# Optimization experiments

Measured on AMD Instinct MI355X. Metric: run time of the kernel, lower is better.

## Reference

```python
import jax, jax.numpy as jnp
import numpy as np

NUM_HEADS = 16
ROPE_THETA = 10000.0


def _rotate_half(x):
    d = x.shape[-1] // 2
    return jnp.concatenate((-x[..., d:], x[..., :d]), axis=-1)


def setup_inputs() -> dict:
    key = jax.random.key(0)
    k1, k2, k3, k4 = jax.random.split(key, 4)
    T, HID = 3072, 1024
    hidden_states = jax.random.normal(k1, (T, HID), dtype=jnp.float32)
    w_qkv = jax.random.normal(k2, (HID, 3 * HID), dtype=jnp.float32) * (1.0 / np.sqrt(HID))
    w_o = jax.random.normal(k3, (HID, HID), dtype=jnp.float32) * (1.0 / np.sqrt(HID))
    attention_mask = jnp.zeros((T, T), dtype=jnp.float32)  # additive bias over token pairs
    position_ids = jax.random.randint(k4, (T,), 0, T, dtype=jnp.int32)
    return {
        "hidden_states": hidden_states,
        "w_qkv": w_qkv,
        "w_o": w_o,
        "attention_mask": attention_mask,
        "position_ids": position_ids,
    }


def reference(hidden_states, w_qkv, w_o, attention_mask, position_ids):
    T, hid = hidden_states.shape
    H = NUM_HEADS
    D = hid // H

    # fused QKV projection (bias=False)
    qkv = hidden_states @ w_qkv  # [T, 3*hid]
    q, k, v = jnp.split(qkv, 3, axis=-1)
    q = q.reshape(T, H, D)
    k = k.reshape(T, H, D)
    v = v.reshape(T, H, D)

    # RoPE per packed-token position_ids
    inv_freq = 1.0 / (ROPE_THETA ** (jnp.arange(0, D, 2, dtype=jnp.float32) / D))  # [D/2]
    freqs = position_ids.astype(jnp.float32)[:, None] * inv_freq[None, :]  # [T, D/2]
    emb = jnp.concatenate((freqs, freqs), axis=-1)  # [T, D]
    cos = jnp.cos(emb)[:, None, :]  # [T, 1, D]
    sin = jnp.sin(emb)[:, None, :]
    q = q * cos + _rotate_half(q) * sin
    k = k * cos + _rotate_half(k) * sin

    # dense token-token attention over packed tokens
    scale = 1.0 / np.sqrt(D).astype(np.float32)
    scores = jnp.einsum("thd,shd->hts", q, k) * scale  # [H, T, T]
    scores = scores + attention_mask[None, :, :]
    probs = jax.nn.softmax(scores, axis=-1)
    out = jnp.einsum("hts,shd->thd", probs, v).reshape(T, hid)
    return out @ w_o
```

## Files before the change

### kernel.cpp

```cpp
#include <hip/hip_runtime.h>
#include <hip/hip_bf16.h>
#include <hip/hip_fp16.h>
#include <math.h>

#define T_TOK 3072
#define HID   1024
#define NH    16
#define HD    64
#define KVSPLIT 4
#define KVCHUNK (T_TOK / KVSPLIT)
#define NQB (T_TOK / 128)
#define LOG2E 1.4426950408889634f

typedef __attribute__((ext_vector_type(8))) short bf16x8;
typedef __attribute__((ext_vector_type(8))) unsigned short u16x8;
typedef __attribute__((ext_vector_type(4))) float f32x4;
typedef __attribute__((ext_vector_type(16))) float f32x16;
typedef __attribute__((ext_vector_type(4))) unsigned int u32x4;

#define VMCNT(n) asm volatile("s_waitcnt vmcnt(" #n ")" ::: "memory")
#define SB() __builtin_amdgcn_sched_barrier(0)

static __device__ __forceinline__ unsigned short f2bf(float x) {
  __hip_bfloat16 h = __float2bfloat16(x);
  return __builtin_bit_cast(unsigned short, h);
}
static __device__ __forceinline__ float bf2f(unsigned short u) {
  unsigned int v = (unsigned int)u << 16;
  return __builtin_bit_cast(float, v);
}
static __device__ __forceinline__ unsigned short f2h(float x) {
  __half h = __float2half(x);
  return __builtin_bit_cast(unsigned short, h);
}
static __device__ __forceinline__ float h2f(unsigned short u) {
  __half h = __builtin_bit_cast(__half, u);
  return __half2float(h);
}
static __device__ __forceinline__ unsigned int pack_bf16(float a, float b) {
  unsigned int ua = __builtin_bit_cast(unsigned int, a) + 0x8000u;
  unsigned int ub = __builtin_bit_cast(unsigned int, b) + 0x8000u;
  return (ua >> 16) | (ub & 0xffff0000u);
}

static __device__ __forceinline__ int swz(int row, int cb) {
  return row * 64 + ((cb ^ ((row & 7) << 4)) >> 1);
}

__global__ __launch_bounds__(256) void prep(const float* __restrict__ X,
                                            const float* __restrict__ Wqkv,
                                            const float* __restrict__ Wo,
                                            const int* __restrict__ pos,
                                            const float* __restrict__ mask,
                                            unsigned short* __restrict__ Xb,
                                            unsigned short* __restrict__ WqkvT,
                                            unsigned short* __restrict__ WoT,
                                            float* __restrict__ ctab,
                                            float* __restrict__ stab,
                                            int* __restrict__ flags) {
  __shared__ float tile[32][33];
  __shared__ int sflag;
  const int b = blockIdx.x;
  const int tid = threadIdx.x;
  if (b < 3072) {
    int i = (b * 256 + tid) * 4;
    float4 v = *(const float4*)(X + i);
    ushort4 o;
    o.x = f2bf(v.x); o.y = f2bf(v.y); o.z = f2bf(v.z); o.w = f2bf(v.w);
    *(ushort4*)(Xb + i) = o;
  } else if (b < 6144) {
    int b2 = b - 3072;
    int c0 = (b2 % 96) * 32, r0 = (b2 / 96) * 32;
    int tx = tid & 31, ty = tid >> 5;
    #pragma unroll
    for (int i2 = 0; i2 < 32; i2 += 8)
      tile[ty + i2][tx] = Wqkv[(size_t)(r0 + ty + i2) * 3072 + c0 + tx];
    __syncthreads();
    #pragma unroll
    for (int i2 = 0; i2 < 32; i2 += 8)
      WqkvT[(size_t)(c0 + ty + i2) * 1024 + r0 + tx] = f2bf(tile[tx][ty + i2]);
  } else if (b < 7168) {
    int b2 = b - 6144;
    int c0 = (b2 % 32) * 32, r0 = (b2 / 32) * 32;
    int tx = tid & 31, ty = tid >> 5;
    #pragma unroll
    for (int i2 = 0; i2 < 32; i2 += 8)
      tile[ty + i2][tx] = Wo[(size_t)(r0 + ty + i2) * 1024 + c0 + tx];
    __syncthreads();
    #pragma unroll
    for (int i2 = 0; i2 < 32; i2 += 8)
      WoT[(size_t)(c0 + ty + i2) * 1024 + r0 + tx] = f2bf(tile[tx][ty + i2]);
  } else if (b < 7552) {
    int i = (b - 7168) * 256 + tid;
    int t = i >> 5, j = i & 31;
    float inv = expf(-(float)j * 0.28782313662425572f);
    float f = (float)pos[t] * inv;
    ctab[i] = cosf(f);
    stab[i] = sinf(f);
  } else {
    int c = b - 7552;
    int qx = c % NQB, z = c / NQB;
    const float* base = mask + (size_t)(qx * 128) * T_TOK + z * KVCHUNK;
    int any = 0;
    const int NC4 = KVCHUNK / 4;
    for (int i = tid; i < 128 * NC4; i += 256) {
      int row = i / NC4, cc = i - row * NC4;
      float4 v = *(const float4*)(base + (size_t)row * T_TOK + cc * 4);
      any |= (v.x != 0.f) | (v.y != 0.f) | (v.z != 0.f) | (v.w != 0.f);
    }
    if (tid == 0) sflag = 0;
    __syncthreads();
    if (__any(any) && (tid & 63) == 0) sflag = 1;
    __syncthreads();
    if (tid == 0) flags[z * NQB + qx] = sflag;
  }
}

__global__ __launch_bounds__(256) void rope_v(const unsigned short* __restrict__ QKVb,
                                              const float* __restrict__ ctab,
                                              const float* __restrict__ stab,
                                              unsigned short* __restrict__ Qh,
                                              unsigned short* __restrict__ Kh,
                                              unsigned short* __restrict__ Vt) {
  const float QSCL = 0.18033688011112042f;
  const int h = blockIdx.y;
  const int t0 = blockIdx.x * 64;
  const int g = threadIdx.x & 3, tl = threadIdx.x >> 2;
  const int t = t0 + tl;
  __shared__ unsigned short vlds[64][72];

  const size_t rowb = (size_t)t * (3 * HID) + h * HD + g * 8;
  u16x8 qa = *(const u16x8*)(QKVb + rowb);
  u16x8 qb = *(const u16x8*)(QKVb + rowb + 32);
  u16x8 ka = *(const u16x8*)(QKVb + rowb + HID);
  u16x8 kb = *(const u16x8*)(QKVb + rowb + HID + 32);
  u16x8 va = *(const u16x8*)(QKVb + rowb + 2 * HID);
  u16x8 vb = *(const u16x8*)(QKVb + rowb + 2 * HID + 32);

  u16x8 qo0, qo1, ko0, ko1;
  #pragma unroll
  for (int e = 0; e < 8; ++e) {
    int j = g * 8 + e;
    float c = ctab[t * 32 + j], s = stab[t * 32 + j];
    float q1 = bf2f(qa[e]), q2 = bf2f(qb[e]);
    float k1 = bf2f(ka[e]), k2 = bf2f(kb[e]);
    qo0[e] = f2bf((q1 * c - q2 * s) * QSCL);
    qo1[e] = f2bf((q2 * c + q1 * s) * QSCL);
    ko0[e] = f2bf(k1 * c - k2 * s);
    ko1[e] = f2bf(k2 * c + k1 * s);
    vlds[tl][j] = va[e];
    vlds[tl][32 + j] = vb[e];
  }
  size_t ob = ((size_t)h * T_TOK + t) * HD + g * 8;
  *(u16x8*)(Qh + ob) = qo0;
  *(u16x8*)(Qh + ob + 32) = qo1;
  *(u16x8*)(Kh + ob) = ko0;
  *(u16x8*)(Kh + ob + 32) = ko1;

  __syncthreads();
  u16x8 o0, o1;
  #pragma unroll
  for (int e = 0; e < 8; ++e) {
    o0[e] = vlds[g * 16 + e][tl];
    o1[e] = vlds[g * 16 + 8 + e][tl];
  }
  u16x8 w0, w1;
  #pragma unroll
  for (int e = 0; e < 4; ++e) {
    w0[e] = o0[e];     w0[4 + e] = o1[e];
    w1[e] = o0[4 + e]; w1[4 + e] = o1[4 + e];
  }
  size_t vb2 = ((size_t)h * HD + tl) * T_TOK + t0 + g * 16;
  *(u16x8*)(Vt + vb2) = w0;
  *(u16x8*)(Vt + vb2 + 8) = w1;
}

template <int OBF16>
__device__ __forceinline__ void gemm_body(const unsigned short* __restrict__ A,
                                          const unsigned short* __restrict__ Bt,
                                          float* __restrict__ C,
                                          unsigned short* __restrict__ Cb,
                                          int M, int N, int K) {
  __shared__ unsigned short As[2][128 * 32];
  __shared__ unsigned short Bs[2][128 * 32];
  const int lane = threadIdx.x & 63;
  const int wv = threadIdx.x >> 6;
  const int wm = wv >> 1, wn = wv & 1;
  const int r = lane & 15, hi = lane >> 4;
  const int nwg = gridDim.x;
  const int flat = blockIdx.x;
  const int sid = (flat & 7) * (nwg >> 3) + (flat >> 3);
  const int mblocks = M >> 7;
  const int m0 = (sid % mblocks) * 128, n0 = (sid / mblocks) * 128;

  const int srow = lane >> 2;
  const int scb  = ((lane & 3) * 16) ^ ((srow & 3) << 4);
  const unsigned short* ga = A  + (size_t)(m0 + wv * 16 + srow) * K + (scb >> 1);
  const unsigned short* gb = Bt + (size_t)(n0 + wv * 16 + srow) * K + (scb >> 1);
  char* asd = (char*)&As[0][0] + wv * 1024;
  char* bsd = (char*)&Bs[0][0] + wv * 1024;

  auto stage = [&](int buf, int kt) {
    __builtin_amdgcn_global_load_lds(
        (const __attribute__((address_space(1))) unsigned int*)(ga + kt),
        (__attribute__((address_space(3))) unsigned int*)(asd + buf * 8192), 16, 0, 0);
    __builtin_amdgcn_global_load_lds(
        (const __attribute__((address_space(1))) unsigned int*)(ga + (size_t)64 * K + kt),
        (__attribute__((address_space(3))) unsigned int*)(asd + buf * 8192 + 4096), 16, 0, 0);
    __builtin_amdgcn_global_load_lds(
        (const __attribute__((address_space(1))) unsigned int*)(gb + kt),
        (__attribute__((address_space(3))) unsigned int*)(bsd + buf * 8192), 16, 0, 0);
    __builtin_amdgcn_global_load_lds(
        (const __attribute__((address_space(1))) unsigned int*)(gb + (size_t)64 * K + kt),
        (__attribute__((address_space(3))) unsigned int*)(bsd + buf * 8192 + 4096), 16, 0, 0);
  };

  f32x4 acc[4][4] = {};
  const int NT = K >> 5;
  stage(0, 0);
  #pragma unroll 2
  for (int it = 0; it < NT; ++it) {
    const int buf = it & 1;
    if (it + 1 < NT) {
      stage(buf ^ 1, (it + 1) * 32);
      VMCNT(4);
    } else {
      VMCNT(0);
    }
    SB();
    __builtin_amdgcn_s_barrier();
    SB();
    bf16x8 a[4], b[4];
    const int cbs = (hi * 16) ^ ((r & 3) << 4);
    #pragma unroll
    for (int tm = 0; tm < 4; ++tm)
      a[tm] = *(const bf16x8*)&As[buf][(wm * 64 + tm * 16 + r) * 32 + (cbs >> 1)];
    #pragma unroll
    for (int tn = 0; tn < 4; ++tn)
      b[tn] = *(const bf16x8*)&Bs[buf][(wn * 64 + tn * 16 + r) * 32 + (cbs >> 1)];
    #pragma unroll
    for (int tm = 0; tm < 4; ++tm)
      #pragma unroll
      for (int tn = 0; tn < 4; ++tn)
        acc[tm][tn] = __builtin_amdgcn_mfma_f32_16x16x32_bf16(a[tm], b[tn], acc[tm][tn], 0, 0, 0);
    __builtin_amdgcn_s_barrier();
  }
  #pragma unroll
  for (int tm = 0; tm < 4; ++tm)
    #pragma unroll
    for (int tn = 0; tn < 4; ++tn) {
      int colg = n0 + wn * 64 + tn * 16 + r;
      int rowg = m0 + wm * 64 + tm * 16 + hi * 4;
      if (OBF16) {
        unsigned short* cp = Cb + (size_t)rowg * N + colg;
        #pragma unroll
        for (int j = 0; j < 4; ++j) cp[(size_t)j * N] = f2bf(acc[tm][tn][j]);
      } else {
        float* cp = C + (size_t)rowg * N + colg;
        #pragma unroll
        for (int j = 0; j < 4; ++j) cp[(size_t)j * N] = acc[tm][tn][j];
      }
    }
}

__global__ __launch_bounds__(256) void gemm_bt(const unsigned short* __restrict__ A,
                                               const unsigned short* __restrict__ Bt,
                                               float* __restrict__ C, int M, int N, int K) {
  gemm_body<0>(A, Bt, C, nullptr, M, N, K);
}
__global__ __launch_bounds__(256) void gemm_bt_bf16(const unsigned short* __restrict__ A,
                                                    const unsigned short* __restrict__ Bt,
                                                    unsigned short* __restrict__ Cb,
                                                    int M, int N, int K) {
  gemm_body<1>(A, Bt, nullptr, Cb, M, N, K);
}

__global__ __launch_bounds__(256) void flash_attn(const unsigned short* __restrict__ Qh,
                                                  const unsigned short* __restrict__ Kh,
                                                  const unsigned short* __restrict__ Vt,
                                                  const float* __restrict__ mask,
                                                  const int* __restrict__ flags,
                                                  unsigned short* __restrict__ Op,
                                                  float* __restrict__ Mp,
                                                  float* __restrict__ Lp) {
  const int NBLK = NH * NQB * KVSPLIT;
  int id = blockIdx.x;
  int sid = (id & 7) * (NBLK / 8) + (id >> 3);
  const int hh = sid / (NQB * KVSPLIT);
  int rem = sid % (NQB * KVSPLIT);
  const int z  = rem / NQB;
  const int qx = rem % NQB;
  const int q0 = qx * 128;
  const int kv0 = z * KVCHUNK;
  const int NT = KVCHUNK / 64;

  __shared__ unsigned short Ks[2][64 * 64];
  __shared__ unsigned short Vs[2][64 * 64];
  const int lane = threadIdx.x & 63, wv = threadIdx.x >> 6;
  const int q31 = lane & 31, h2 = lane >> 5;
  const int qw = q0 + wv * 32 + q31;

  bf16x8 qf[4];
  #pragma unroll
  for (int ks = 0; ks < 4; ++ks)
    qf[ks] = *(const bf16x8*)(Qh + ((size_t)hh * T_TOK + qw) * HD + ks * 16 + h2 * 8);

  f32x16 acc_o[2] = {};
  const int hasmask = flags[z * NQB + qx];
  float m = hasmask ? -INFINITY : 0.f;
  float l = 0.f;

  const int ldrow = lane >> 3;
  const int colS  = ((lane & 7) * 16) ^ (ldrow << 4);
  const unsigned short* kga = Kh + ((size_t)hh * T_TOK + wv * 16 + ldrow) * HD + (colS >> 1);
  const unsigned short* vga = Vt + ((size_t)hh * HD + wv * 16 + ldrow) * T_TOK + (colS >> 1);
  char* ksd = (char*)&Ks[0][0] + wv * 2048;
  char* vsd = (char*)&Vs[0][0] + wv * 2048;
  const float* mrow = mask + (size_t)qw * T_TOK;

  auto stage = [&](int buf, int s0) {
    __builtin_amdgcn_global_load_lds(
        (const __attribute__((address_space(1))) unsigned int*)(kga + (size_t)s0 * HD),
        (__attribute__((address_space(3))) unsigned int*)(ksd + buf * 8192), 16, 0, 0);
    __builtin_amdgcn_global_load_lds(
        (const __attribute__((address_space(1))) unsigned int*)(kga + (size_t)s0 * HD + 8 * HD),
        (__attribute__((address_space(3))) unsigned int*)(ksd + buf * 8192 + 1024), 16, 0, 0);
    __builtin_amdgcn_global_load_lds(
        (const __attribute__((address_space(1))) unsigned int*)(vga + s0),
        (__attribute__((address_space(3))) unsigned int*)(vsd + buf * 8192), 16, 0, 0);
    __builtin_amdgcn_global_load_lds(
        (const __attribute__((address_space(1))) unsigned int*)(vga + s0 + 8 * T_TOK),
        (__attribute__((address_space(3))) unsigned int*)(vsd + buf * 8192 + 1024), 16, 0, 0);
  };

  float4 mk[8];

  auto qkt = [&](int cur, f32x16& as0, f32x16& as1) {
    __builtin_amdgcn_s_setprio(1);
    #pragma unroll
    for (int ks = 0; ks < 4; ++ks) {
      bf16x8 kf0 = *(const bf16x8*)&Ks[cur][swz(q31,      ks * 32 + h2 * 16)];
      bf16x8 kf1 = *(const bf16x8*)&Ks[cur][swz(32 + q31, ks * 32 + h2 * 16)];
      as0 = __builtin_amdgcn_mfma_f32_32x32x16_bf16(kf0, qf[ks], as0, 0, 0, 0);
      as1 = __builtin_amdgcn_mfma_f32_32x32x16_bf16(kf1, qf[ks], as1, 0, 0, 0);
    }
    __builtin_amdgcn_s_setprio(0);
  };

  auto pv = [&](int cur, const unsigned int* pk) {
    __builtin_amdgcn_s_setprio(1);
    #pragma unroll
    for (int kvb = 0; kvb < 2; ++kvb)
      #pragma unroll
      for (int s = 0; s < 2; ++s) {
        u32x4 fr;
        fr[0] = pk[kvb * 8 + 4 * s + 0];
        fr[1] = pk[kvb * 8 + 4 * s + 1];
        fr[2] = pk[kvb * 8 + 4 * s + 2];
        fr[3] = pk[kvb * 8 + 4 * s + 3];
        bf16x8 pfrag = __builtin_bit_cast(bf16x8, fr);
        #pragma unroll
        for (int db = 0; db < 2; ++db) {
          bf16x8 vf = *(const bf16x8*)&Vs[cur][swz(db * 32 + q31, kvb * 64 + s * 32 + h2 * 16)];
          acc_o[db] = __builtin_amdgcn_mfma_f32_32x32x16_bf16(vf, pfrag, acc_o[db], 0, 0, 0);
        }
      }
    __builtin_amdgcn_s_setprio(0);
  };

  auto tile_nomask = [&](int cur) {
    f32x16 as0 = {}, as1 = {};
    qkt(cur, as0, as1);
    float ps = 0.f;
    unsigned int pk[16];
    #pragma unroll
    for (int kvb = 0; kvb < 2; ++kvb) {
      const f32x16& as = kvb ? as1 : as0;
      #pragma unroll
      for (int j = 0; j < 4; ++j) {
        float e0 = __builtin_amdgcn_exp2f(as[j * 4 + 0]);
        float e1 = __builtin_amdgcn_exp2f(as[j * 4 + 1]);
        float e2 = __builtin_amdgcn_exp2f(as[j * 4 + 2]);
        float e3 = __builtin_amdgcn_exp2f(as[j * 4 + 3]);
        ps += (e0 + e1) + (e2 + e3);
        pk[kvb * 8 + j * 2 + 0] = pack_bf16(e0, e1);
        pk[kvb * 8 + j * 2 + 1] = pack_bf16(e2, e3);
      }
    }
    l += ps;
    pv(cur, pk);
  };

  auto tile_mask = [&](int cur) {
    f32x16 as0 = {}, as1 = {};
    qkt(cur, as0, as1);
    float sv[2][16];
    #pragma unroll
    for (int reg = 0; reg < 16; ++reg) {
      float m0v = (&mk[0 + (reg >> 2)].x)[reg & 3];
      float m1v = (&mk[4 + (reg >> 2)].x)[reg & 3];
      sv[0][reg] = fmaf(m0v, LOG2E, as0[reg]);
      sv[1][reg] = fmaf(m1v, LOG2E, as1[reg]);
    }
    float p0 = sv[0][0];
    #pragma unroll
    for (int i = 1; i < 16; ++i) p0 = fmaxf(p0, sv[0][i]);
    #pragma unroll
    for (int i = 0; i < 16; ++i) p0 = fmaxf(p0, sv[1][i]);
    float pmax = fmaxf(p0, __shfl_xor(p0, 32));
    if (__any(pmax > m + 8.f)) {
      float mnew = fmaxf(m, pmax);
      float sc = __builtin_amdgcn_exp2f(m - mnew);
      m = mnew;
      l *= sc;
      #pragma unroll
      for (int db = 0; db < 2; ++db)
        #pragma unroll
        for (int i = 0; i < 16; ++i) acc_o[db][i] *= sc;
    }
    float ps = 0.f;
    unsigned int pk[16];
    #pragma unroll
    for (int kvb = 0; kvb < 2; ++kvb)
      #pragma unroll
      for (int j = 0; j < 4; ++j) {
        float e0 = __builtin_amdgcn_exp2f(sv[kvb][j * 4 + 0] - m);
        float e1 = __builtin_amdgcn_exp2f(sv[kvb][j * 4 + 1] - m);
        float e2 = __builtin_amdgcn_exp2f(sv[kvb][j * 4 + 2] - m);
        float e3 = __builtin_amdgcn_exp2f(sv[kvb][j * 4 + 3] - m);
        ps += (e0 + e1) + (e2 + e3);
        pk[kvb * 8 + j * 2 + 0] = pack_bf16(e0, e1);
        pk[kvb * 8 + j * 2 + 1] = pack_bf16(e2, e3);
      }
    l += ps;
    pv(cur, pk);
  };

  stage(0, kv0);

  if (hasmask) {
    for (int it = 0; it < NT - 1; ++it) {
      const int s0 = kv0 + it * 64;
      #pragma unroll
      for (int kvb = 0; kvb < 2; ++kvb)
        #pragma unroll
        for (int g = 0; g < 4; ++g)
          mk[kvb * 4 + g] = *(const float4*)(mrow + s0 + kvb * 32 + g * 8 + 4 * h2);
      stage((it + 1) & 1, s0 + 64);
      VMCNT(12);
      SB();
      __builtin_amdgcn_s_barrier();
      SB();
      tile_mask(it & 1);
      __builtin_amdgcn_s_barrier();
    }
    const int s0 = kv0 + (NT - 1) * 64;
    #pragma unroll
    for (int kvb = 0; kvb < 2; ++kvb)
      #pragma unroll
      for (int g = 0; g < 4; ++g)
        mk[kvb * 4 + g] = *(const float4*)(mrow + s0 + kvb * 32 + g * 8 + 4 * h2);
    VMCNT(8);
    SB();
    __builtin_amdgcn_s_barrier();
    SB();
    tile_mask((NT - 1) & 1);
  } else {
    for (int it = 0; it < NT - 1; ++it) {
      stage((it + 1) & 1, kv0 + (it + 1) * 64);
      VMCNT(4);
      SB();
      __builtin_amdgcn_s_barrier();
      SB();
      tile_nomask(it & 1);
      __builtin_amdgcn_s_barrier();
    }
    VMCNT(0);
    SB();
    __builtin_amdgcn_s_barrier();
    SB();
    tile_nomask((NT - 1) & 1);
  }

  float lf = l + __shfl_xor(l, 32);
  float lfinv = 1.f / lf;
  unsigned short* oprow = Op + (((size_t)z * T_TOK + qw) * NH + hh) * HD;
  #pragma unroll
  for (int db = 0; db < 2; ++db)
    #pragma unroll
    for (int g = 0; g < 4; ++g) {
      ushort4 o4;
      o4.x = f2h(acc_o[db][g * 4 + 0] * lfinv);
      o4.y = f2h(acc_o[db][g * 4 + 1] * lfinv);
      o4.z = f2h(acc_o[db][g * 4 + 2] * lfinv);
      o4.w = f2h(acc_o[db][g * 4 + 3] * lfinv);
      *(ushort4*)(oprow + db * 32 + g * 8 + 4 * h2) = o4;
    }
  if (h2 == 0) {
    size_t mi = ((size_t)z * T_TOK + qw) * NH + hh;
    Mp[mi] = m;
    Lp[mi] = lf;
  }
}

__global__ __launch_bounds__(256) void combine(const unsigned short* __restrict__ Op,
                                               const float* __restrict__ Mp,
                                               const float* __restrict__ Lp,
                                               unsigned short* __restrict__ Ob) {
  int idx = blockIdx.x * 256 + threadIdx.x;
  int t = idx >> 8;
  int q4 = (idx & 255) * 4;
  int h = q4 >> 6, d = q4 & 63;
  float mz[KVSPLIT], lz[KVSPLIT];
  float ms = -INFINITY;
  #pragma unroll
  for (int zz = 0; zz < KVSPLIT; ++zz) {
    size_t mi = ((size_t)zz * T_TOK + t) * NH + h;
    mz[zz] = Mp[mi];
    lz[zz] = Lp[mi];
    ms = fmaxf(ms, mz[zz]);
  }
  float lsum = 0.f;
  float wl[KVSPLIT];
  #pragma unroll
  for (int zz = 0; zz < KVSPLIT; ++zz) {
    wl[zz] = lz[zz] * __builtin_amdgcn_exp2f(mz[zz] - ms);
    lsum += wl[zz];
  }
  float4 o = {0.f, 0.f, 0.f, 0.f};
  #pragma unroll
  for (int zz = 0; zz < KVSPLIT; ++zz) {
    ushort4 p = *(const ushort4*)(Op + (((size_t)zz * T_TOK + t) * NH + h) * HD + d);
    o.x += h2f(p.x) * wl[zz]; o.y += h2f(p.y) * wl[zz];
    o.z += h2f(p.z) * wl[zz]; o.w += h2f(p.w) * wl[zz];
  }
  float inv = 1.f / lsum;
  ushort4 ob;
  ob.x = f2bf(o.x * inv); ob.y = f2bf(o.y * inv);
  ob.z = f2bf(o.z * inv); ob.w = f2bf(o.w * inv);
  *(ushort4*)(Ob + (size_t)t * HID + q4) = ob;
}

extern "C" void kernel_launch(void* const* d_in, const int* in_sizes, int n_in,
                              void* d_out, int out_size, void* d_ws, size_t ws_size,
                              hipStream_t stream) {
  const float* X    = (const float*)d_in[0];
  const float* Wqkv = (const float*)d_in[1];
  const float* Wo   = (const float*)d_in[2];
  const float* mask = (const float*)d_in[3];
  const int*   pos  = (const int*)d_in[4];
  float* out = (float*)d_out;

  char* ws = (char*)d_ws;
  size_t off = 0;
  auto alloc = [&](size_t bytes) {
    char* p = ws + off;
    off += (bytes + 255) & ~(size_t)255;
    return p;
  };
  unsigned short* Xb    = (unsigned short*)alloc((size_t)T_TOK * HID * 2);
  unsigned short* WqkvT = (unsigned short*)alloc((size_t)3 * HID * HID * 2);
  unsigned short* WoT   = (unsigned short*)alloc((size_t)HID * HID * 2);
  unsigned short* Qh    = (unsigned short*)alloc((size_t)NH * T_TOK * HD * 2);
  unsigned short* Kh    = (unsigned short*)alloc((size_t)NH * T_TOK * HD * 2);
  unsigned short* Vt    = (unsigned short*)alloc((size_t)NH * HD * T_TOK * 2);
  unsigned short* Ob    = (unsigned short*)alloc((size_t)T_TOK * HID * 2);
  float*          ctab  = (float*)alloc((size_t)T_TOK * 32 * 4);
  float*          stab  = (float*)alloc((size_t)T_TOK * 32 * 4);
  float*          Mp    = (float*)alloc((size_t)KVSPLIT * T_TOK * NH * 4);
  float*          Lp    = (float*)alloc((size_t)KVSPLIT * T_TOK * NH * 4);
  int*            flags = (int*)alloc((size_t)KVSPLIT * NQB * 4);
  char*           region = alloc((size_t)KVSPLIT * T_TOK * HID * 2);
  unsigned short* QKVb  = (unsigned short*)region;
  unsigned short* Op    = (unsigned short*)region;

  prep<<<7648, 256, 0, stream>>>(X, Wqkv, Wo, pos, mask, Xb, WqkvT, WoT, ctab, stab, flags);

  gemm_bt_bf16<<<dim3((3 * HID / 128) * (T_TOK / 128)), 256, 0, stream>>>(Xb, WqkvT, QKVb, T_TOK, 3 * HID, HID);

  rope_v<<<dim3(T_TOK / 64, NH), 256, 0, stream>>>(QKVb, ctab, stab, Qh, Kh, Vt);

  flash_attn<<<dim3(NH * NQB * KVSPLIT), 256, 0, stream>>>(Qh, Kh, Vt, mask, flags, Op, Mp, Lp);
  combine<<<T_TOK, 256, 0, stream>>>(Op, Mp, Lp, Ob);

  gemm_bt<<<dim3((HID / 128) * (T_TOK / 128)), 256, 0, stream>>>(Ob, WoT, out, T_TOK, HID, HID);
}
```

Baseline: 156.2 us.

## Fuse RoPE, Q scaling and V transpose into the QKV GEMM epilogue

Removes the separate rope_v kernel and the intermediate bf16 QKV buffer. The QKV GEMM epilogue now applies RoPE, using cos/sin tables staged into the reused LDS, writes head-major Q and K directly, and stores V transposed. This saves one launch and a full write and read of the QKV intermediate. In exchange the epilogue stores become scattered 2-byte writes for Q/K and 8-byte writes for V, which may coalesce poorly.

```diff
diff --git a/kernel.cpp b/kernel.cpp
--- a/kernel.cpp
+++ b/kernel.cpp
@@ -116,71 +116,14 @@
   }
 }
 
-__global__ __launch_bounds__(256) void rope_v(const unsigned short* __restrict__ QKVb,
-                                              const float* __restrict__ ctab,
-                                              const float* __restrict__ stab,
-                                              unsigned short* __restrict__ Qh,
-                                              unsigned short* __restrict__ Kh,
-                                              unsigned short* __restrict__ Vt) {
-  const float QSCL = 0.18033688011112042f;
-  const int h = blockIdx.y;
-  const int t0 = blockIdx.x * 64;
-  const int g = threadIdx.x & 3, tl = threadIdx.x >> 2;
-  const int t = t0 + tl;
-  __shared__ unsigned short vlds[64][72];
-
-  const size_t rowb = (size_t)t * (3 * HID) + h * HD + g * 8;
-  u16x8 qa = *(const u16x8*)(QKVb + rowb);
-  u16x8 qb = *(const u16x8*)(QKVb + rowb + 32);
-  u16x8 ka = *(const u16x8*)(QKVb + rowb + HID);
-  u16x8 kb = *(const u16x8*)(QKVb + rowb + HID + 32);
-  u16x8 va = *(const u16x8*)(QKVb + rowb + 2 * HID);
-  u16x8 vb = *(const u16x8*)(QKVb + rowb + 2 * HID + 32);
-
-  u16x8 qo0, qo1, ko0, ko1;
-  #pragma unroll
-  for (int e = 0; e < 8; ++e) {
-    int j = g * 8 + e;
-    float c = ctab[t * 32 + j], s = stab[t * 32 + j];
-    float q1 = bf2f(qa[e]), q2 = bf2f(qb[e]);
-    float k1 = bf2f(ka[e]), k2 = bf2f(kb[e]);
-    qo0[e] = f2bf((q1 * c - q2 * s) * QSCL);
-    qo1[e] = f2bf((q2 * c + q1 * s) * QSCL);
-    ko0[e] = f2bf(k1 * c - k2 * s);
-    ko1[e] = f2bf(k2 * c + k1 * s);
-    vlds[tl][j] = va[e];
-    vlds[tl][32 + j] = vb[e];
-  }
-  size_t ob = ((size_t)h * T_TOK + t) * HD + g * 8;
-  *(u16x8*)(Qh + ob) = qo0;
-  *(u16x8*)(Qh + ob + 32) = qo1;
-  *(u16x8*)(Kh + ob) = ko0;
-  *(u16x8*)(Kh + ob + 32) = ko1;
-
-  __syncthreads();
-  u16x8 o0, o1;
-  #pragma unroll
-  for (int e = 0; e < 8; ++e) {
-    o0[e] = vlds[g * 16 + e][tl];
-    o1[e] = vlds[g * 16 + 8 + e][tl];
-  }
-  u16x8 w0, w1;
-  #pragma unroll
-  for (int e = 0; e < 4; ++e) {
-    w0[e] = o0[e];     w0[4 + e] = o1[e];
-    w1[e] = o0[4 + e]; w1[4 + e] = o1[4 + e];
-  }
-  size_t vb2 = ((size_t)h * HD + tl) * T_TOK + t0 + g * 16;
-  *(u16x8*)(Vt + vb2) = w0;
-  *(u16x8*)(Vt + vb2 + 8) = w1;
-}
-
-template <int OBF16>
-__device__ __forceinline__ void gemm_body(const unsigned short* __restrict__ A,
-                                          const unsigned short* __restrict__ Bt,
-                                          float* __restrict__ C,
-                                          unsigned short* __restrict__ Cb,
-                                          int M, int N, int K) {
+__global__ __launch_bounds__(256) void gemm_qkv(const unsigned short* __restrict__ A,
+                                                const unsigned short* __restrict__ Bt,
+                                                const float* __restrict__ ctab,
+                                                const float* __restrict__ stab,
+                                                unsigned short* __restrict__ Qh,
+                                                unsigned short* __restrict__ Kh,
+                                                unsigned short* __restrict__ Vt) {
+  const int M = T_TOK, N = 3 * HID, K = HID;
   __shared__ unsigned short As[2][128 * 32];
   __shared__ unsigned short Bs[2][128 * 32];
   const int lane = threadIdx.x & 63;
@@ -245,34 +188,129 @@
         acc[tm][tn] = __builtin_amdgcn_mfma_f32_16x16x32_bf16(a[tm], b[tn], acc[tm][tn], 0, 0, 0);
     __builtin_amdgcn_s_barrier();
   }
+
+  const int sec = n0 >> 10;
+  const int hh  = ((n0 + wn * 64) >> 6) & 15;
+  if (sec < 2) {
+    __syncthreads();
+    float* ctl = (float*)&As[0][0];
+    float* stl = (float*)&Bs[0][0];
+    for (int i = threadIdx.x; i < 1024; i += 256) {
+      ((float4*)ctl)[i] = *(const float4*)(ctab + (size_t)m0 * 32 + i * 4);
+      ((float4*)stl)[i] = *(const float4*)(stab + (size_t)m0 * 32 + i * 4);
+    }
+    __syncthreads();
+    const float qscl = (sec == 0) ? 0.18033688011112042f : 1.0f;
+    unsigned short* dst = (sec == 0) ? Qh : Kh;
+    #pragma unroll
+    for (int tm = 0; tm < 4; ++tm)
+      #pragma unroll
+      for (int tn2 = 0; tn2 < 2; ++tn2) {
+        const int p = tn2 * 16 + r;
+        #pragma unroll
+        for (int j = 0; j < 4; ++j) {
+          int trow = wm * 64 + tm * 16 + hi * 4 + j;
+          float c = ctl[trow * 32 + p], s = stl[trow * 32 + p];
+          float q1 = acc[tm][tn2][j], q2 = acc[tm][tn2 + 2][j];
+          size_t base = ((size_t)hh * T_TOK + (m0 + trow)) * HD + p;
+          dst[base]      = f2bf((q1 * c - q2 * s) * qscl);
+          dst[base + 32] = f2bf((q2 * c + q1 * s) * qscl);
+        }
+      }
+  } else {
+    const int hi2 = ((hi & 1) << 1) | (hi >> 1);
+    #pragma unroll
+    for (int tn = 0; tn < 4; ++tn) {
+      const int d = tn * 16 + r;
+      #pragma unroll
+      for (int tm = 0; tm < 4; ++tm) {
+        int tbase = m0 + wm * 64 + tm * 16 + hi2 * 4;
+        ushort4 w;
+        w.x = f2bf(acc[tm][tn][0]); w.y = f2bf(acc[tm][tn][1]);
+        w.z = f2bf(acc[tm][tn][2]); w.w = f2bf(acc[tm][tn][3]);
+        *(ushort4*)(Vt + ((size_t)hh * HD + d) * T_TOK + tbase) = w;
+      }
+    }
+  }
+}
+
+__global__ __launch_bounds__(256) void gemm_bt(const unsigned short* __restrict__ A,
+                                               const unsigned short* __restrict__ Bt,
+                                               float* __restrict__ C, int M, int N, int K) {
+  __shared__ unsigned short As[2][128 * 32];
+  __shared__ unsigned short Bs[2][128 * 32];
+  const int lane = threadIdx.x & 63;
+  const int wv = threadIdx.x >> 6;
+  const int wm = wv >> 1, wn = wv & 1;
+  const int r = lane & 15, hi = lane >> 4;
+  const int nwg = gridDim.x;
+  const int flat = blockIdx.x;
+  const int sid = (flat & 7) * (nwg >> 3) + (flat >> 3);
+  const int mblocks = M >> 7;
+  const int m0 = (sid % mblocks) * 128, n0 = (sid / mblocks) * 128;
+
+  const int srow = lane >> 2;
+  const int scb  = ((lane & 3) * 16) ^ ((srow & 3) << 4);
+  const unsigned short* ga = A  + (size_t)(m0 + wv * 16 + srow) * K + (scb >> 1);
+  const unsigned short* gb = Bt + (size_t)(n0 + wv * 16 + srow) * K + (scb >> 1);
+  char* asd = (char*)&As[0][0] + wv * 1024;
+  char* bsd = (char*)&Bs[0][0] + wv * 1024;
+
+  auto stage = [&](int buf, int kt) {
+    __builtin_amdgcn_global_load_lds(
+        (const __attribute__((address_space(1))) unsigned int*)(ga + kt),
+        (__attribute__((address_space(3))) unsigned int*)(asd + buf * 8192), 16, 0, 0);
+    __builtin_amdgcn_global_load_lds(
+        (const __attribute__((address_space(1))) unsigned int*)(ga + (size_t)64 * K + kt),
+        (__attribute__((address_space(3))) unsigned int*)(asd + buf * 8192 + 4096), 16, 0, 0);
+    __builtin_amdgcn_global_load_lds(
+        (const __attribute__((address_space(1))) unsigned int*)(gb + kt),
+        (__attribute__((address_space(3))) unsigned int*)(bsd + buf * 8192), 16, 0, 0);
+    __builtin_amdgcn_global_load_lds(
+        (const __attribute__((address_space(1))) unsigned int*)(gb + (size_t)64 * K + kt),
+        (__attribute__((address_space(3))) unsigned int*)(bsd + buf * 8192 + 4096), 16, 0, 0);
+  };
+
+  f32x4 acc[4][4] = {};
+  const int NT = K >> 5;
+  stage(0, 0);
+  #pragma unroll 2
+  for (int it = 0; it < NT; ++it) {
+    const int buf = it & 1;
+    if (it + 1 < NT) {
+      stage(buf ^ 1, (it + 1) * 32);
+      VMCNT(4);
+    } else {
+      VMCNT(0);
+    }
+    SB();
+    __builtin_amdgcn_s_barrier();
+    SB();
+    bf16x8 a[4], b[4];
+    const int cbs = (hi * 16) ^ ((r & 3) << 4);
+    #pragma unroll
+    for (int tm = 0; tm < 4; ++tm)
+      a[tm] = *(const bf16x8*)&As[buf][(wm * 64 + tm * 16 + r) * 32 + (cbs >> 1)];
+    #pragma unroll
+    for (int tn = 0; tn < 4; ++tn)
+      b[tn] = *(const bf16x8*)&Bs[buf][(wn * 64 + tn * 16 + r) * 32 + (cbs >> 1)];
+    #pragma unroll
+    for (int tm = 0; tm < 4; ++tm)
+      #pragma unroll
+      for (int tn = 0; tn < 4; ++tn)
+        acc[tm][tn] = __builtin_amdgcn_mfma_f32_16x16x32_bf16(a[tm], b[tn], acc[tm][tn], 0, 0, 0);
+    __builtin_amdgcn_s_barrier();
+  }
   #pragma unroll
   for (int tm = 0; tm < 4; ++tm)
     #pragma unroll
     for (int tn = 0; tn < 4; ++tn) {
       int colg = n0 + wn * 64 + tn * 16 + r;
       int rowg = m0 + wm * 64 + tm * 16 + hi * 4;
-      if (OBF16) {
-        unsigned short* cp = Cb + (size_t)rowg * N + colg;
-        #pragma unroll
-        for (int j = 0; j < 4; ++j) cp[(size_t)j * N] = f2bf(acc[tm][tn][j]);
-      } else {
-        float* cp = C + (size_t)rowg * N + colg;
-        #pragma unroll
-        for (int j = 0; j < 4; ++j) cp[(size_t)j * N] = acc[tm][tn][j];
-      }
-    }
-}
-
-__global__ __launch_bounds__(256) void gemm_bt(const unsigned short* __restrict__ A,
-                                               const unsigned short* __restrict__ Bt,
-                                               float* __restrict__ C, int M, int N, int K) {
-  gemm_body<0>(A, Bt, C, nullptr, M, N, K);
-}
-__global__ __launch_bounds__(256) void gemm_bt_bf16(const unsigned short* __restrict__ A,
-                                                    const unsigned short* __restrict__ Bt,
-                                                    unsigned short* __restrict__ Cb,
-                                                    int M, int N, int K) {
-  gemm_body<1>(A, Bt, nullptr, Cb, M, N, K);
+      float* cp = C + (size_t)rowg * N + colg;
+      #pragma unroll
+      for (int j = 0; j < 4; ++j) cp[(size_t)j * N] = acc[tm][tn][j];
+    }
 }
 
 __global__ __launch_bounds__(256) void flash_attn(const unsigned short* __restrict__ Qh,
@@ -570,15 +608,11 @@
   float*          Mp    = (float*)alloc((size_t)KVSPLIT * T_TOK * NH * 4);
   float*          Lp    = (float*)alloc((size_t)KVSPLIT * T_TOK * NH * 4);
   int*            flags = (int*)alloc((size_t)KVSPLIT * NQB * 4);
-  char*           region = alloc((size_t)KVSPLIT * T_TOK * HID * 2);
-  unsigned short* QKVb  = (unsigned short*)region;
-  unsigned short* Op    = (unsigned short*)region;
+  unsigned short* Op    = (unsigned short*)alloc((size_t)KVSPLIT * T_TOK * HID * 2);
 
   prep<<<7648, 256, 0, stream>>>(X, Wqkv, Wo, pos, mask, Xb, WqkvT, WoT, ctab, stab, flags);
 
-  gemm_bt_bf16<<<dim3((3 * HID / 128) * (T_TOK / 128)), 256, 0, stream>>>(Xb, WqkvT, QKVb, T_TOK, 3 * HID, HID);
-
-  rope_v<<<dim3(T_TOK / 64, NH), 256, 0, stream>>>(QKVb, ctab, stab, Qh, Kh, Vt);
+  gemm_qkv<<<dim3((3 * HID / 128) * (T_TOK / 128)), 256, 0, stream>>>(Xb, WqkvT, ctab, stab, Qh, Kh, Vt);
 
   flash_attn<<<dim3(NH * NQB * KVSPLIT), 256, 0, stream>>>(Qh, Kh, Vt, mask, flags, Op, Mp, Lp);
   combine<<<T_TOK, 256, 0, stream>>>(Op, Mp, Lp, Ob);
```

Measured after the change: 152.1 us. 2.6% less time.
